# Kernel optimization log

Hardware: AMD Instinct MI355X
Metric: run time of the kernel (lower is better)

Reference implementation:

```python
import jax, jax.numpy as jnp
import numpy as np

B, F, T, K = 16, 256, 1024, 10


def setup_inputs() -> dict:
    key = jax.random.key(0)
    k1, k2, k3, k4, k5 = jax.random.split(key, 5)
    mu = jax.random.normal(k1, (B, F, T, K), dtype=jnp.float32)
    log_std = jax.random.normal(k2, (B, F, T, K), dtype=jnp.float32)
    pi_logits = jax.random.normal(k3, (B, F, T, K), dtype=jnp.float32)
    u_cat = jax.random.uniform(k4, (B, F, T), dtype=jnp.float32)
    eps = jax.random.normal(k5, (B, F, T), dtype=jnp.float32)
    return {"mu": mu, "log_std": log_std, "pi_logits": pi_logits,
            "u_cat": u_cat, "eps": eps}


def reference(mu, log_std, pi_logits, u_cat, eps):
    # GMM per-pixel sampling (sample_gmm_batch):
    #   pi  = softmax(pi_logits)                  mixture weights
    #   k   = categorical(pi) via inverse-CDF using uniform u_cat
    #   out = mu[k] + exp(log_std[k]) * eps       reparameterized normal draw
    pi = jax.nn.softmax(pi_logits, axis=-1)              # [B,F,T,K]
    cdf = jnp.cumsum(pi, axis=-1)                        # [B,F,T,K]
    # component index: number of cdf entries strictly below u
    k_idx = jnp.sum(cdf < u_cat[..., None], axis=-1)     # [B,F,T]
    k_idx = jnp.clip(k_idx, 0, K - 1)
    mu_k = jnp.take_along_axis(mu, k_idx[..., None], axis=-1)[..., 0]
    ls_k = jnp.take_along_axis(log_std, k_idx[..., None], axis=-1)[..., 0]
    out = mu_k + jnp.exp(ls_k) * eps                     # [B,F,T]
    return out
```

## Files before the change

kernel.cpp:

```cpp
#include <hip/hip_runtime.h>
#include <math.h>


#define KMIX 10
#define TPB 128
#define PX_PER_BLOCK (TPB * 2)
#define F_PER_ARRAY (PX_PER_BLOCK * KMIX)
#define F4_PER_ARRAY (F_PER_ARRAY / 4)

__device__ __forceinline__ int compute_k(const float* lt, float uval) {
    float m = lt[0];
    #pragma unroll
    for (int j = 1; j < KMIX; ++j) m = fmaxf(m, lt[j]);

    float e[KMIX];
    float S = 0.f;
    #pragma unroll
    for (int j = 0; j < KMIX; ++j) {
        e[j] = expf(lt[j] - m);
        S += e[j];
    }

    float cdf = 0.f;
    int k = 0;
    #pragma unroll
    for (int j = 0; j < KMIX; ++j) {
        cdf += e[j] / S;
        k += (cdf < uval) ? 1 : 0;
    }
    return (k > KMIX - 1) ? (KMIX - 1) : k;
}

__global__ __launch_bounds__(TPB, 4) void gmm_sample_kernel(
    const float* __restrict__ mu,
    const float* __restrict__ log_std,
    const float* __restrict__ pi_logits,
    const float* __restrict__ u_cat,
    const float* __restrict__ eps,
    float* __restrict__ out,
    int npairs)
{
    __shared__ float4 sA[F4_PER_ARRAY];
    __shared__ float4 sB[F4_PER_ARRAY];

    const int tid = threadIdx.x;
    const size_t blk = blockIdx.x;
    const size_t base_f4 = blk * F4_PER_ARRAY;

    const float4* gpi = reinterpret_cast<const float4*>(pi_logits) + base_f4;
    const float4* gmu = reinterpret_cast<const float4*>(mu)        + base_f4;
    const float4* gls = reinterpret_cast<const float4*>(log_std)   + base_f4;

    float4 tp[5];
    #pragma unroll
    for (int j = 0; j < 5; ++j) tp[j] = gpi[j * TPB + tid];

    const size_t pair = blk * TPB + tid;
    float2 uu = reinterpret_cast<const float2*>(u_cat)[pair];
    float2 ee = reinterpret_cast<const float2*>(eps)[pair];

    #pragma unroll
    for (int j = 0; j < 5; ++j) sA[j * TPB + tid] = tp[j];
    __syncthreads();

    float4 tm[5], tl[5];
    #pragma unroll
    for (int j = 0; j < 5; ++j) tm[j] = gmu[j * TPB + tid];
    #pragma unroll
    for (int j = 0; j < 5; ++j) tl[j] = gls[j * TPB + tid];

    float l[2 * KMIX];
    #pragma unroll
    for (int j = 0; j < 5; ++j) {
        float4 a = sA[tid * 5 + j];
        l[4 * j + 0] = a.x; l[4 * j + 1] = a.y;
        l[4 * j + 2] = a.z; l[4 * j + 3] = a.w;
    }

    int k0 = compute_k(l, uu.x);
    int k1 = compute_k(l + KMIX, uu.y);

    __syncthreads();

    #pragma unroll
    for (int j = 0; j < 5; ++j) sA[j * TPB + tid] = tm[j];
    #pragma unroll
    for (int j = 0; j < 5; ++j) sB[j * TPB + tid] = tl[j];
    __syncthreads();

    const float* s_mu = reinterpret_cast<const float*>(sA);
    const float* s_ls = reinterpret_cast<const float*>(sB);
    float mk0 = s_mu[20 * tid + k0];
    float sk0 = s_ls[20 * tid + k0];
    float mk1 = s_mu[20 * tid + KMIX + k1];
    float sk1 = s_ls[20 * tid + KMIX + k1];

    float2 r;
    r.x = mk0 + expf(sk0) * ee.x;
    r.y = mk1 + expf(sk1) * ee.y;
    if (pair < (size_t)npairs)
        reinterpret_cast<float2*>(out)[pair] = r;
}

extern "C" void kernel_launch(void* const* d_in, const int* in_sizes, int n_in,
                              void* d_out, int out_size, void* d_ws, size_t ws_size,
                              hipStream_t stream) {
    const float* mu        = (const float*)d_in[0];
    const float* log_std   = (const float*)d_in[1];
    const float* pi_logits = (const float*)d_in[2];
    const float* u_cat     = (const float*)d_in[3];
    const float* eps       = (const float*)d_in[4];
    float* out = (float*)d_out;

    int N = in_sizes[3];
    int npairs = N / 2;
    int grid = (npairs + TPB - 1) / TPB;
    gmm_sample_kernel<<<grid, TPB, 0, stream>>>(mu, log_std, pi_logits,
                                                u_cat, eps, out, npairs);
}
```

Baseline: 499.1 us.

## Load mixture tiles directly into LDS and defer the mu fetch

```diff
diff --git a/kernel.cpp b/kernel.cpp
--- a/kernel.cpp
+++ b/kernel.cpp
@@ -1,12 +1,18 @@
 #include <hip/hip_runtime.h>
 #include <math.h>
+#include <stdint.h>
 
 
 #define KMIX 10
 #define TPB 128
-#define PX_PER_BLOCK (TPB * 2)
-#define F_PER_ARRAY (PX_PER_BLOCK * KMIX)
-#define F4_PER_ARRAY (F_PER_ARRAY / 4)
+#define F4_PER_ARRAY 640
+
+__device__ __forceinline__ void gload_lds16(const float4* g, float4* l) {
+    __builtin_amdgcn_global_load_lds(
+        (const __attribute__((address_space(1))) void*)g,
+        (__attribute__((address_space(3))) void*)l,
+        16, 0, 0);
+}
 
 __device__ __forceinline__ int compute_k(const float* lt, float uval) {
     float m = lt[0];
@@ -51,23 +57,17 @@
     const float4* gmu = reinterpret_cast<const float4*>(mu)        + base_f4;
     const float4* gls = reinterpret_cast<const float4*>(log_std)   + base_f4;
 
-    float4 tp[5];
     #pragma unroll
-    for (int j = 0; j < 5; ++j) tp[j] = gpi[j * TPB + tid];
+    for (int j = 0; j < 5; ++j) gload_lds16(gpi + j * TPB + tid, &sA[j * TPB + tid]);
+    #pragma unroll
+    for (int j = 0; j < 5; ++j) gload_lds16(gls + j * TPB + tid, &sB[j * TPB + tid]);
 
     const size_t pair = blk * TPB + tid;
     float2 uu = reinterpret_cast<const float2*>(u_cat)[pair];
     float2 ee = reinterpret_cast<const float2*>(eps)[pair];
 
-    #pragma unroll
-    for (int j = 0; j < 5; ++j) sA[j * TPB + tid] = tp[j];
+    asm volatile("s_waitcnt vmcnt(0)" ::: "memory");
     __syncthreads();
-
-    float4 tm[5], tl[5];
-    #pragma unroll
-    for (int j = 0; j < 5; ++j) tm[j] = gmu[j * TPB + tid];
-    #pragma unroll
-    for (int j = 0; j < 5; ++j) tl[j] = gls[j * TPB + tid];
 
     float l[2 * KMIX];
     #pragma unroll
@@ -80,24 +80,28 @@
     int k0 = compute_k(l, uu.x);
     int k1 = compute_k(l + KMIX, uu.y);
 
+    const float* s_ls = reinterpret_cast<const float*>(sB);
+    float sk0 = s_ls[20 * tid + k0];
+    float sk1 = s_ls[20 * tid + KMIX + k1];
+
     __syncthreads();
 
     #pragma unroll
-    for (int j = 0; j < 5; ++j) sA[j * TPB + tid] = tm[j];
-    #pragma unroll
-    for (int j = 0; j < 5; ++j) sB[j * TPB + tid] = tl[j];
+    for (int j = 0; j < 5; ++j) gload_lds16(gmu + j * TPB + tid, &sA[j * TPB + tid]);
+
+    float t0 = expf(sk0) * ee.x;
+    float t1 = expf(sk1) * ee.y;
+
+    asm volatile("s_waitcnt vmcnt(0)" ::: "memory");
     __syncthreads();
 
     const float* s_mu = reinterpret_cast<const float*>(sA);
-    const float* s_ls = reinterpret_cast<const float*>(sB);
     float mk0 = s_mu[20 * tid + k0];
-    float sk0 = s_ls[20 * tid + k0];
     float mk1 = s_mu[20 * tid + KMIX + k1];
-    float sk1 = s_ls[20 * tid + KMIX + k1];
 
     float2 r;
-    r.x = mk0 + expf(sk0) * ee.x;
-    r.y = mk1 + expf(sk1) * ee.y;
+    r.x = mk0 + t0;
+    r.y = mk1 + t1;
     if (pair < (size_t)npairs)
         reinterpret_cast<float2*>(out)[pair] = r;
 }
```

Measured after the change: 454.1 us. 1.1x faster.
